# Performance work log

Measured on AMD Instinct MI355X. Metric: run time of the kernel, lower is better.

## Reference

```python
import jax, jax.numpy as jnp
import numpy as np
import math

B, T, NEURAL = 8, 8192, 256
D, H, L, FF = 1024, 16, 8, 4096
HD = D // H
KLEN = 14
BLANK = 41
DIP = 40
INTER = 3
GKS, GSIG = 20, 2.0
DAYS = 24


def _gauss_kernel():
    x = np.arange(GKS, dtype=np.float32)
    mean = (GKS - 1) / 2
    k = np.exp(-(((x - mean) / GSIG) ** 2) / 2) / (GSIG * math.sqrt(2 * math.pi))
    k = k / k.sum()
    return jnp.asarray(np.tile(k[None, None, :], (NEURAL, 1, 1)))  # [C,1,K]


def _ln(x, w, b, eps=1e-5):
    mu = jnp.mean(x, axis=-1, keepdims=True)
    xc = x - mu
    var = jnp.mean(xc * xc, axis=-1, keepdims=True)
    return xc * jax.lax.rsqrt(var + eps) * w + b


def setup_inputs() -> dict:
    key = jax.random.key(0)
    ks = iter(jax.random.split(key, 64))
    def nrm(shape, s=0.02):
        return jax.random.normal(next(ks), shape, jnp.float32) * s
    PE_IN = KLEN * NEURAL
    return {
        "neural": jax.random.normal(next(ks), (B, T, NEURAL), jnp.float32),
        "lengths": jax.random.randint(next(ks), (B,), 1, T + 1),
        "day_idx": jax.random.randint(next(ks), (B,), 0, DAYS),
        "day_W": jnp.broadcast_to(jnp.eye(NEURAL, dtype=jnp.float32), (DAYS, NEURAL, NEURAL)) + nrm((DAYS, NEURAL, NEURAL), 0.01),
        "day_b": jnp.zeros((DAYS, 1, NEURAL), jnp.float32),
        "pe_ln1_w": jnp.ones((PE_IN,), jnp.float32),
        "pe_ln1_b": jnp.zeros((PE_IN,), jnp.float32),
        "pe_W": nrm((PE_IN, D)),
        "pe_b": jnp.zeros((D,), jnp.float32),
        "pe_ln2_w": jnp.ones((D,), jnp.float32),
        "pe_ln2_b": jnp.zeros((D,), jnp.float32),
        "ln_attn_w": jnp.ones((L, D), jnp.float32),
        "ln_attn_b": jnp.zeros((L, D), jnp.float32),
        "qkv_W": nrm((L, D, 3 * D)),
        "qkv_b": jnp.zeros((L, 3 * D), jnp.float32),
        "attn_out_W": nrm((L, D, D)),
        "attn_out_b": jnp.zeros((L, D), jnp.float32),
        "ff_ln_w": jnp.ones((L, D), jnp.float32),
        "ff_ln_b": jnp.zeros((L, D), jnp.float32),
        "fc1_W": nrm((L, D, FF)),
        "fc1_b": jnp.zeros((L, FF), jnp.float32),
        "fc2_W": nrm((L, FF, D)),
        "fc2_b": jnp.zeros((L, D), jnp.float32),
        "final_ln_w": jnp.ones((D,), jnp.float32),
        "final_ln_b": jnp.zeros((D,), jnp.float32),
        "ih_W": nrm((D, BLANK)),
        "ih_b": jnp.zeros((BLANK,), jnp.float32),
        "fb_W": nrm((BLANK, D)),
        "fb_b": jnp.zeros((D,), jnp.float32),
        "fh_W": nrm((D, BLANK)),
        "fh_b": jnp.zeros((BLANK,), jnp.float32),
        "dh_W": nrm((D, DIP * DIP)),
        "dh_b": jnp.zeros((DIP * DIP,), jnp.float32),
    }


def reference(neural, lengths, day_idx, day_W, day_b, pe_ln1_w, pe_ln1_b, pe_W, pe_b, pe_ln2_w, pe_ln2_b, ln_attn_w, ln_attn_b, qkv_W, qkv_b, attn_out_W, attn_out_b, ff_ln_w, ff_ln_b, fc1_W, fc1_b, fc2_W, fc2_b, final_ln_w, final_ln_b, ih_W, ih_b, fb_W, fb_b, fh_W, fh_b, dh_W, dh_b):
    # --- depthwise gaussian smoothing along time (even kernel -> length T+1, as torch) ---
    x = jnp.transpose(neural, (0, 2, 1))  # [B, C, T]
    x = jax.lax.conv_general_dilated(x, _gauss_kernel(), (1,), [(GKS // 2, GKS // 2)],
                                     dimension_numbers=("NCH", "OIH", "NCH"),
                                     feature_group_count=NEURAL)
    x = jnp.transpose(x, (0, 2, 1))  # [B, T+1, C]
    # --- day-specific linear + softsign + length mask ---
    x = jnp.einsum("btd,bdk->btk", x, day_W[day_idx]) + day_b[day_idx]
    x = x / (1.0 + jnp.abs(x))  # Softsign
    Tm = x.shape[1]
    pm = jnp.arange(Tm)[None, :] >= lengths[:, None]
    x = jnp.where(pm[:, :, None], 0.0, x)
    # --- patch embedding ---
    npatch = Tm // KLEN
    x = x[:, : npatch * KLEN, :].reshape(B, npatch, KLEN * NEURAL)
    x = _ln(x, pe_ln1_w, pe_ln1_b, 1e-6)
    x = x @ pe_W + pe_b
    x = _ln(x, pe_ln2_w, pe_ln2_b, 1e-6)
    S = npatch
    causal = jnp.triu(jnp.full((S, S), -1e9, dtype=x.dtype), 1)
    eff = jnp.maximum(lengths // KLEN, 1)
    pad = jnp.arange(S)[None, :] >= eff[:, None]  # [B, S]
    scale = 1.0 / math.sqrt(HD)
    h = x
    inter_lp = None
    for i in range(L):
        a = _ln(h, ln_attn_w[i], ln_attn_b[i])
        qkv = a @ qkv_W[i] + qkv_b[i]
        q, k, v = jnp.split(qkv, 3, axis=-1)
        q = q.reshape(B, S, H, HD).transpose(0, 2, 1, 3)
        k = k.reshape(B, S, H, HD).transpose(0, 2, 1, 3)
        v = v.reshape(B, S, H, HD).transpose(0, 2, 1, 3)
        sc = jnp.einsum("bhqd,bhkd->bhqk", q, k) * scale + causal
        sc = jnp.where(pad[:, None, None, :], -1e30, sc)
        att = jax.nn.softmax(sc, axis=-1)
        o = jnp.einsum("bhqk,bhkd->bhqd", att, v).transpose(0, 2, 1, 3).reshape(B, S, D)
        o = o @ attn_out_W[i] + attn_out_b[i]
        o = jnp.where(pad[:, :, None], 0.0, o)
        h = h + o
        f = _ln(h, ff_ln_w[i], ff_ln_b[i])
        f = jax.nn.gelu(f @ fc1_W[i] + fc1_b[i], approximate=False) @ fc2_W[i] + fc2_b[i]
        h = h + f
        if i == INTER:
            inter_lp = jax.nn.log_softmax(h @ ih_W + ih_b, axis=-1)
            h = h + (jnp.exp(inter_lp) @ fb_W + fb_b)  # feedback projection
    h = _ln(h, final_ln_w, final_ln_b)
    final_lp = jax.nn.log_softmax(h @ fh_W + fh_b, axis=-1)
    # --- diphone marginalization ---
    lp = jax.nn.log_softmax(h @ dh_W + dh_b, axis=-1).reshape(B, S, DIP, DIP)
    left = jax.scipy.special.logsumexp(lp, axis=3)
    right = jax.scipy.special.logsumexp(lp, axis=2)
    comb = jnp.logaddexp(left, right) - math.log(2.0)
    comb = comb - jax.scipy.special.logsumexp(comb, axis=-1, keepdims=True)
    return final_lp, inter_lp, comb
```

## Files before the change

### kernel.cpp

```cpp
#include <hip/hip_runtime.h>
#include <math.h>

#define Bz    8
#define Tt    8192
#define NEU   256
#define Dm    1024
#define Hh    16
#define Ll    8
#define FFd   4096
#define HDd   64
#define KL    14
#define BLANK 41
#define DIPd  40
#define GKS   20
#define TmD   8193
#define Ss    585
#define PEIN  3584
#define MTOK  (Bz * Ss)
#define SpV   608
#define TCH   128

#define NEG_INF (-3.4e38f)

typedef __attribute__((ext_vector_type(8))) short short8;
typedef __attribute__((ext_vector_type(4))) float f32x4;
typedef unsigned short ushort_t;

__device__ __forceinline__ float bf2f(ushort_t u) {
  union { unsigned int i; float f; } v; v.i = ((unsigned int)u) << 16; return v.f;
}
__device__ __forceinline__ ushort_t f2bf(float f) {
  union { float f; unsigned int i; } v; v.f = f;
  unsigned int x = v.i;
  if ((x & 0x7fffffffu) > 0x7f800000u) return 0x7fc0;
  return (ushort_t)((x + 0x7fffu + ((x >> 16) & 1u)) >> 16);
}

__global__ __launch_bounds__(256) void smooth_kernel(
    const float* __restrict__ neural, float* __restrict__ out) {
  const int b = blockIdx.y, c = threadIdx.x;
  const int t0 = blockIdx.x * TCH;
  float w[GKS];
  float wsum = 0.f;
#pragma unroll
  for (int j = 0; j < GKS; j++) {
    float e = (j - 9.5f) * 0.5f;
    w[j] = expf(-0.5f * e * e);
    wsum += w[j];
  }
  const float inv = 1.f / wsum;
#pragma unroll
  for (int j = 0; j < GKS; j++) w[j] *= inv;

  const float* src = neural + (size_t)b * Tt * NEU + c;
  float* dst = out + ((size_t)b * TmD + t0) * NEU + c;

  float win[GKS];
#pragma unroll
  for (int j = 0; j < GKS; j++) {
    const int tt = t0 - GKS / 2 + j;
    win[j] = (tt >= 0 && tt < Tt) ? src[(size_t)tt * NEU] : 0.f;
  }
  const int nt = min(TCH, TmD - t0);
  for (int t = 0; t < nt; t++) {
    const int tt = t0 + t + GKS / 2;
    const float nv = (tt < Tt) ? src[(size_t)tt * NEU] : 0.f;
    float acc = 0.f;
#pragma unroll
    for (int j = 0; j < GKS; j++) acc += win[j] * w[j];
    dst[(size_t)t * NEU] = acc;
#pragma unroll
    for (int j = 0; j < GKS - 1; j++) win[j] = win[j + 1];
    win[GKS - 1] = nv;
  }
}

#define DROWS 16
__global__ __launch_bounds__(256) void day_kernel(
    float* __restrict__ x, const float* __restrict__ dayW,
    const float* __restrict__ dayB, const int* __restrict__ day_idx,
    const int* __restrict__ lengths) {
  const int b = blockIdx.y;
  const int t0 = blockIdx.x * DROWS;
  const int c = threadIdx.x;
  const int di = day_idx[b];
  const int len = lengths[b];
  const float* W = dayW + (size_t)di * NEU * NEU;
  __shared__ float rows[DROWS][NEU];
  float* xb = x + ((size_t)b * TmD + t0) * NEU;
  const int nr = min(DROWS, TmD - t0);
  for (int r = 0; r < nr; r++) rows[r][c] = xb[(size_t)r * NEU + c];
  __syncthreads();
  float acc[DROWS];
  const float bb = dayB[(size_t)di * NEU + c];
#pragma unroll
  for (int r = 0; r < DROWS; r++) acc[r] = bb;
  for (int d = 0; d < NEU; d++) {
    const float w = W[(size_t)d * NEU + c];
#pragma unroll
    for (int r = 0; r < DROWS; r++) acc[r] += rows[r][d] * w;
  }
  for (int r = 0; r < nr; r++) {
    const int t = t0 + r;
    float v = acc[r] / (1.f + fabsf(acc[r]));
    xb[(size_t)r * NEU + c] = (t < len) ? v : 0.f;
  }
}

__global__ __launch_bounds__(256) void ln_kernel(
    const float* __restrict__ in, const float* __restrict__ w,
    const float* __restrict__ bias, float* __restrict__ dstf,
    ushort_t* __restrict__ dstb,
    int N, float eps, int inner, long strideA, long strideB) {
  const int row = blockIdx.x;
  const float* src = in + (size_t)(row / inner) * strideA + (size_t)(row % inner) * strideB;
  const int tid = threadIdx.x;
  float s = 0.f, ss = 0.f;
  for (int i = tid; i < N; i += 256) {
    float v = src[i];
    s += v; ss += v * v;
  }
  __shared__ float rs[256], rss[256];
  rs[tid] = s; rss[tid] = ss;
  __syncthreads();
  for (int k = 128; k > 0; k >>= 1) {
    if (tid < k) { rs[tid] += rs[tid + k]; rss[tid] += rss[tid + k]; }
    __syncthreads();
  }
  const float mean = rs[0] / N;
  const float var = rss[0] / N - mean * mean;
  const float rstd = rsqrtf(var + eps);
  for (int i = tid; i < N; i += 256) {
    const float r = (src[i] - mean) * rstd * w[i] + bias[i];
    if (dstf) dstf[(size_t)row * N + i] = r;
    else dstb[(size_t)row * N + i] = f2bf(r);
  }
}

__global__ __launch_bounds__(256) void convt_kernel(
    const float* __restrict__ in, ushort_t* __restrict__ out,
    int R, int C, int Rp) {
  __shared__ float t[32][33];
  const int r0 = blockIdx.x * 32, c0 = blockIdx.y * 32;
  const int tx = threadIdx.x, ty = threadIdx.y;
#pragma unroll
  for (int i = 0; i < 4; i++) {
    const int r = r0 + ty + i * 8, c = c0 + tx;
    t[ty + i * 8][tx] = (r < R && c < C) ? in[(size_t)r * C + c] : 0.f;
  }
  __syncthreads();
#pragma unroll
  for (int i = 0; i < 4; i++) {
    const int c = c0 + ty + i * 8, r = r0 + tx;
    if (c < C && r < Rp) out[(size_t)c * Rp + r] = f2bf(t[tx][ty + i * 8]);
  }
}

__global__ __launch_bounds__(256) void f2b_kernel(
    const float* __restrict__ in, ushort_t* __restrict__ out, int n) {
  for (int i = blockIdx.x * 256 + threadIdx.x; i < n; i += gridDim.x * 256)
    out[i] = f2bf(in[i]);
}

#define BM 128
#define BN 128
#define BKh 32
__global__ __launch_bounds__(256) void gemm_bf16(
    const ushort_t* __restrict__ A, const ushort_t* __restrict__ Bt,
    const float* __restrict__ bias, float* __restrict__ Cf,
    ushort_t* __restrict__ Cb, int M, int N, int K, int epi,
    const int* __restrict__ eff) {
  __shared__ short As[BM * BKh];
  __shared__ short Bs[BN * BKh];
  const int tid = threadIdx.x;
  const int wave = tid >> 6, lane = tid & 63;
  const int lm = lane & 15, quad = lane >> 4;
  const int bm = blockIdx.x * BM, bn = blockIdx.y * BN;
  const int wm = (wave >> 1) * 64, wn = (wave & 1) * 64;

  f32x4 acc[4][4] = {};

  const int ldrow = lane >> 2;
  const int ldk = (lane & 3) * 8;

  for (int k0 = 0; k0 < K; k0 += BKh) {
#pragma unroll
    for (int r = 0; r < 4; r++) {
      const int cid = wave * 4 + r;
      if (cid < 8) {
        int row = bm + cid * 16 + ldrow;
        row = min(row, M - 1);
        const ushort_t* gp = A + (size_t)row * K + k0 + ldk;
        __builtin_amdgcn_global_load_lds(
            (const __attribute__((address_space(1))) unsigned int*)gp,
            (__attribute__((address_space(3))) unsigned int*)((char*)As + cid * 1024),
            16, 0, 0);
      } else {
        int row = bn + (cid - 8) * 16 + ldrow;
        row = min(row, N - 1);
        const ushort_t* gp = Bt + (size_t)row * K + k0 + ldk;
        __builtin_amdgcn_global_load_lds(
            (const __attribute__((address_space(1))) unsigned int*)gp,
            (__attribute__((address_space(3))) unsigned int*)((char*)Bs + (cid - 8) * 1024),
            16, 0, 0);
      }
    }
    __syncthreads();
    short8 af[4], bf[4];
#pragma unroll
    for (int mt = 0; mt < 4; mt++)
      af[mt] = *(const short8*)&As[(wm + mt * 16 + lm) * BKh + quad * 8];
#pragma unroll
    for (int nt = 0; nt < 4; nt++)
      bf[nt] = *(const short8*)&Bs[(wn + nt * 16 + lm) * BKh + quad * 8];
#pragma unroll
    for (int mt = 0; mt < 4; mt++)
#pragma unroll
      for (int nt = 0; nt < 4; nt++)
        acc[mt][nt] = __builtin_amdgcn_mfma_f32_16x16x32_bf16(
            af[mt], bf[nt], acc[mt][nt], 0, 0, 0);
    __syncthreads();
  }

#pragma unroll
  for (int mt = 0; mt < 4; mt++) {
#pragma unroll
    for (int r = 0; r < 4; r++) {
      const int gm = bm + wm + mt * 16 + quad * 4 + r;
      if (gm >= M) continue;
      bool masked = false;
      if (epi == 3) masked = ((gm % Ss) >= eff[gm / Ss]);
#pragma unroll
      for (int nt = 0; nt < 4; nt++) {
        const int gn = bn + wn + nt * 16 + lm;
        if (gn >= N) continue;
        const float v = acc[mt][nt][r] + bias[gn];
        const size_t o = (size_t)gm * N + gn;
        if (epi == 0) Cf[o] = v;
        else if (epi == 1) Cb[o] = f2bf(0.5f * v * (1.f + erff(v * 0.70710678118654752f)));
        else if (epi == 2) Cf[o] += v;
        else if (epi == 3) { if (!masked) Cf[o] += v; }
        else Cb[o] = f2bf(v);
      }
    }
  }
}

__global__ __launch_bounds__(256) void vt_kernel(
    const ushort_t* __restrict__ qkv, ushort_t* __restrict__ vt) {
  __shared__ ushort_t t[32][33];
  const int s0 = blockIdx.x * 32;
  const int h = blockIdx.y >> 1, d0 = (blockIdx.y & 1) * 32;
  const int b = blockIdx.z;
  const int tx = threadIdx.x, ty = threadIdx.y;
#pragma unroll
  for (int i = 0; i < 4; i++) {
    const int s = s0 + ty + i * 8;
    t[ty + i * 8][tx] = (s < Ss)
        ? qkv[((size_t)(b * Ss + s) * 3 + 2) * Dm + h * HDd + d0 + tx]
        : (ushort_t)0;
  }
  __syncthreads();
#pragma unroll
  for (int i = 0; i < 4; i++) {
    const int d = d0 + ty + i * 8;
    vt[((size_t)(b * Hh + h) * HDd + d) * SpV + s0 + tx] = t[tx][ty + i * 8];
  }
}

__global__ __launch_bounds__(256) void fattn_kernel(
    const ushort_t* __restrict__ qkv, const ushort_t* __restrict__ vt,
    ushort_t* __restrict__ out, const int* __restrict__ eff) {
  const int wave = threadIdx.x >> 6, lane = threadIdx.x & 63;
  const int lm = lane & 15, quad = lane >> 4;
  const int nQT = (Ss + 15) / 16;
  const int qt = ((int)gridDim.x - 1 - (int)blockIdx.x) * 4 + wave;
  if (qt >= nQT) return;
  const int h = blockIdx.y, b = blockIdx.z;
  const int e = eff[b];
  __shared__ ushort_t pl[4][16][40];
  const int q0 = qt * 16;

  const int qrow = min(q0 + lm, Ss - 1);
  const short8* qp = (const short8*)(qkv + (size_t)(b * Ss + qrow) * 3 * Dm + h * HDd + quad * 8);
  const short8 aq0 = qp[0], aq1 = qp[4];

  f32x4 acc[4] = {};
  float mrow[4], lrow[4];
#pragma unroll
  for (int r = 0; r < 4; r++) { mrow[r] = NEG_INF; lrow[r] = 0.f; }

  const int kmax = min(q0 + 15, e - 1);
  const int ntiles = (kmax >> 5) + 1;

  for (int kt = 0; kt < ntiles; kt++) {
    const int k0 = kt * 32;
    f32x4 s0 = {}, s1 = {};
    {
      const int c = min(k0 + lm, Ss - 1);
      const short8* kp = (const short8*)(qkv + ((size_t)(b * Ss + c) * 3 + 1) * Dm + h * HDd + quad * 8);
      s0 = __builtin_amdgcn_mfma_f32_16x16x32_bf16(aq0, kp[0], s0, 0, 0, 0);
      s0 = __builtin_amdgcn_mfma_f32_16x16x32_bf16(aq1, kp[4], s0, 0, 0, 0);
    }
    {
      const int c = min(k0 + 16 + lm, Ss - 1);
      const short8* kp = (const short8*)(qkv + ((size_t)(b * Ss + c) * 3 + 1) * Dm + h * HDd + quad * 8);
      s1 = __builtin_amdgcn_mfma_f32_16x16x32_bf16(aq0, kp[0], s1, 0, 0, 0);
      s1 = __builtin_amdgcn_mfma_f32_16x16x32_bf16(aq1, kp[4], s1, 0, 0, 0);
    }
    float sv0[4], sv1[4], tm[4];
#pragma unroll
    for (int r = 0; r < 4; r++) {
      const int row = q0 + quad * 4 + r;
      const int jm = min(row, e - 1);
      sv0[r] = (k0 + lm <= jm) ? s0[r] * 0.125f : NEG_INF;
      sv1[r] = (k0 + 16 + lm <= jm) ? s1[r] * 0.125f : NEG_INF;
      tm[r] = fmaxf(sv0[r], sv1[r]);
    }
#pragma unroll
    for (int off = 8; off; off >>= 1)
#pragma unroll
      for (int r = 0; r < 4; r++) tm[r] = fmaxf(tm[r], __shfl_xor(tm[r], off));
    float ps[4];
#pragma unroll
    for (int r = 0; r < 4; r++) {
      const float nm = fmaxf(mrow[r], tm[r]);
      const float sc = expf(mrow[r] - nm);
      mrow[r] = nm;
      const float p0 = expf(sv0[r] - nm);
      const float p1 = expf(sv1[r] - nm);
      sv0[r] = p0; sv1[r] = p1;
      ps[r] = p0 + p1;
      lrow[r] *= sc;
#pragma unroll
      for (int nt = 0; nt < 4; nt++) acc[nt][r] *= sc;
    }
#pragma unroll
    for (int off = 8; off; off >>= 1)
#pragma unroll
      for (int r = 0; r < 4; r++) ps[r] += __shfl_xor(ps[r], off);
#pragma unroll
    for (int r = 0; r < 4; r++) {
      lrow[r] += ps[r];
      pl[wave][quad * 4 + r][lm] = f2bf(sv0[r]);
      pl[wave][quad * 4 + r][16 + lm] = f2bf(sv1[r]);
    }
    const short8 pf = *(const short8*)&pl[wave][lm][quad * 8];
    const ushort_t* vtb = vt + (size_t)(b * Hh + h) * HDd * SpV + k0 + quad * 8;
#pragma unroll
    for (int nt = 0; nt < 4; nt++) {
      const short8 vf = *(const short8*)(vtb + (size_t)(nt * 16 + lm) * SpV);
      acc[nt] = __builtin_amdgcn_mfma_f32_16x16x32_bf16(pf, vf, acc[nt], 0, 0, 0);
    }
  }

#pragma unroll
  for (int r = 0; r < 4; r++) {
    const int row = q0 + quad * 4 + r;
    if (row >= Ss) continue;
    const float inv = 1.f / lrow[r];
#pragma unroll
    for (int nt = 0; nt < 4; nt++)
      out[(size_t)(b * Ss + row) * Dm + h * HDd + nt * 16 + lm] = f2bf(acc[nt][r] * inv);
  }
}

__global__ __launch_bounds__(64) void lsm41_kernel(
    const float* __restrict__ in, float* __restrict__ lp,
    ushort_t* __restrict__ probs) {
  const int row = blockIdx.x, t = threadIdx.x;
  const float z = (t < BLANK) ? in[(size_t)row * BLANK + t] : NEG_INF;
  float m = z;
#pragma unroll
  for (int off = 32; off; off >>= 1) m = fmaxf(m, __shfl_xor(m, off));
  float s = (t < BLANK) ? expf(z - m) : 0.f;
#pragma unroll
  for (int off = 32; off; off >>= 1) s += __shfl_xor(s, off);
  const float l = z - m - logf(s);
  if (t < BLANK) lp[(size_t)row * BLANK + t] = l;
  if (probs) probs[(size_t)row * 64 + t] = (t < BLANK) ? f2bf(expf(l)) : 0;
}

__global__ __launch_bounds__(64) void diphone_kernel(
    const float* __restrict__ in, float* __restrict__ out) {
  __shared__ float z[DIPd * DIPd];
  __shared__ float u[DIPd];
  const int row = blockIdx.x, t = threadIdx.x;
  for (int i = t; i < DIPd * DIPd; i += 64) z[i] = in[(size_t)row * (DIPd * DIPd) + i];
  __syncthreads();
  if (t < DIPd) {
    float m1 = NEG_INF;
    for (int j = 0; j < DIPd; j++) m1 = fmaxf(m1, z[t * DIPd + j]);
    float s1 = 0.f;
    for (int j = 0; j < DIPd; j++) s1 += expf(z[t * DIPd + j] - m1);
    const float lr = m1 + logf(s1);
    float m2 = NEG_INF;
    for (int j = 0; j < DIPd; j++) m2 = fmaxf(m2, z[j * DIPd + t]);
    float s2 = 0.f;
    for (int j = 0; j < DIPd; j++) s2 += expf(z[j * DIPd + t] - m2);
    const float lc = m2 + logf(s2);
    const float mx = fmaxf(lr, lc), mn = fminf(lr, lc);
    u[t] = mx + log1pf(expf(mn - mx));
  }
  __syncthreads();
  const float v = (t < DIPd) ? u[t] : NEG_INF;
  float m = v;
#pragma unroll
  for (int off = 32; off; off >>= 1) m = fmaxf(m, __shfl_xor(m, off));
  float s = (t < DIPd) ? expf(v - m) : 0.f;
#pragma unroll
  for (int off = 32; off; off >>= 1) s += __shfl_xor(s, off);
  const float lse = m + logf(s);
  if (t < DIPd) out[(size_t)row * DIPd + t] = v - lse;
}

__global__ void eff_kernel(const int* __restrict__ lengths, int* __restrict__ eff) {
  const int t = threadIdx.x;
  if (t < Bz) {
    int e = lengths[t] / KL;
    eff[t] = e < 1 ? 1 : e;
  }
}

extern "C" void kernel_launch(void* const* d_in, const int* in_sizes, int n_in,
                              void* d_out, int out_size, void* d_ws, size_t ws_size,
                              hipStream_t stream) {
  (void)in_sizes; (void)n_in; (void)out_size; (void)ws_size;
  const float* neural     = (const float*)d_in[0];
  const int*   lengths    = (const int*)d_in[1];
  const int*   day_idx    = (const int*)d_in[2];
  const float* day_W      = (const float*)d_in[3];
  const float* day_b      = (const float*)d_in[4];
  const float* pe_ln1_w   = (const float*)d_in[5];
  const float* pe_ln1_b   = (const float*)d_in[6];
  const float* pe_W       = (const float*)d_in[7];
  const float* pe_b       = (const float*)d_in[8];
  const float* pe_ln2_w   = (const float*)d_in[9];
  const float* pe_ln2_b   = (const float*)d_in[10];
  const float* ln_attn_w  = (const float*)d_in[11];
  const float* ln_attn_b  = (const float*)d_in[12];
  const float* qkv_W      = (const float*)d_in[13];
  const float* qkv_b      = (const float*)d_in[14];
  const float* attn_out_W = (const float*)d_in[15];
  const float* attn_out_b = (const float*)d_in[16];
  const float* ff_ln_w    = (const float*)d_in[17];
  const float* ff_ln_b    = (const float*)d_in[18];
  const float* fc1_W      = (const float*)d_in[19];
  const float* fc1_b      = (const float*)d_in[20];
  const float* fc2_W      = (const float*)d_in[21];
  const float* fc2_b      = (const float*)d_in[22];
  const float* final_ln_w = (const float*)d_in[23];
  const float* final_ln_b = (const float*)d_in[24];
  const float* ih_W       = (const float*)d_in[25];
  const float* ih_b       = (const float*)d_in[26];
  const float* fb_W       = (const float*)d_in[27];
  const float* fb_b       = (const float*)d_in[28];
  const float* fh_W       = (const float*)d_in[29];
  const float* fh_b       = (const float*)d_in[30];
  const float* dh_W       = (const float*)d_in[31];
  const float* dh_b       = (const float*)d_in[32];

  float* out = (float*)d_out;
  char* p = (char*)d_ws;

  float*    buf_x    = (float*)p;          p += 67117056;
  ushort_t* buf_pein = (ushort_t*)p;
  ushort_t* buf_qkv  = (ushort_t*)p;       p += 33546240;
  float*    buf_h    = (float*)p;          p += 19169280;
  ushort_t* buf_abf  = (ushort_t*)p;       p += 9584640;
  ushort_t* buf_ao   = (ushort_t*)p;       p += 9584640;
  char*     ffp      = p;                  p += 38338560;
  ushort_t* wbuf     = (ushort_t*)p;       p += 25380864;
  int*      eff      = (int*)p;            p += 32;

  ushort_t* buf_ff   = (ushort_t*)ffp;
  float*    buf_dip  = (float*)ffp;
  float*    buf_blank= (float*)(ffp + 29952000);
  ushort_t* buf_probs= (ushort_t*)(ffp + 30719520);
  float*    buf_peout= buf_x;
  ushort_t* buf_vt   = (ushort_t*)buf_x;

  ushort_t* qkvT = wbuf;
  ushort_t* aoT  = wbuf + 3145728;
  ushort_t* fc1T = wbuf + 4194304;
  ushort_t* fc2T = wbuf + 8388608;
  ushort_t* ihT  = wbuf + 12582912;
  ushort_t* fbT  = wbuf + 12624896;
  ushort_t* peT  = wbuf;
  ushort_t* dhT  = wbuf;
  ushort_t* fhT  = wbuf + 1638400;

  auto convt = [&](const float* in, ushort_t* o, int R, int C, int Rp) {
    dim3 g((Rp + 31) / 32, (C + 31) / 32);
    convt_kernel<<<g, dim3(32, 8), 0, stream>>>(in, o, R, C, Rp);
  };
  auto gemm = [&](const ushort_t* A, const ushort_t* Bt, const float* bias,
                  float* Cf, ushort_t* Cb, int M_, int N_, int K_, int epi) {
    dim3 g((M_ + BM - 1) / BM, (N_ + BN - 1) / BN);
    gemm_bf16<<<g, 256, 0, stream>>>(A, Bt, bias, Cf, Cb, M_, N_, K_, epi, eff);
  };

  eff_kernel<<<1, 64, 0, stream>>>(lengths, eff);
  smooth_kernel<<<dim3((TmD + TCH - 1) / TCH, Bz), 256, 0, stream>>>(neural, buf_x);
  day_kernel<<<dim3((TmD + DROWS - 1) / DROWS, Bz), 256, 0, stream>>>(buf_x, day_W, day_b, day_idx, lengths);

  ln_kernel<<<MTOK, 256, 0, stream>>>(buf_x, pe_ln1_w, pe_ln1_b, nullptr, buf_pein,
                                      PEIN, 1e-6f, Ss, (long)TmD * NEU, (long)KL * NEU);
  convt(pe_W, peT, PEIN, Dm, PEIN);
  convt(ih_W, ihT, Dm, BLANK, Dm);
  convt(fb_W, fbT, BLANK, Dm, 64);
  gemm(buf_pein, peT, pe_b, buf_peout, nullptr, MTOK, Dm, PEIN, 0);
  ln_kernel<<<MTOK, 256, 0, stream>>>(buf_peout, pe_ln2_w, pe_ln2_b, buf_h, nullptr,
                                      Dm, 1e-6f, MTOK, 0L, (long)Dm);

  const int nQT = (Ss + 15) / 16;
  const int fgx = (nQT + 3) / 4;

  for (int i = 0; i < Ll; i++) {
    convt(qkv_W + (size_t)i * Dm * 3 * Dm, qkvT, Dm, 3 * Dm, Dm);
    convt(attn_out_W + (size_t)i * Dm * Dm, aoT, Dm, Dm, Dm);
    convt(fc1_W + (size_t)i * Dm * FFd, fc1T, Dm, FFd, Dm);
    convt(fc2_W + (size_t)i * FFd * Dm, fc2T, FFd, Dm, FFd);

    ln_kernel<<<MTOK, 256, 0, stream>>>(buf_h, ln_attn_w + (size_t)i * Dm,
                                        ln_attn_b + (size_t)i * Dm, nullptr, buf_abf,
                                        Dm, 1e-5f, MTOK, 0L, (long)Dm);
    gemm(buf_abf, qkvT, qkv_b + (size_t)i * 3 * Dm, nullptr, buf_qkv,
         MTOK, 3 * Dm, Dm, 4);
    vt_kernel<<<dim3(SpV / 32, Hh * 2, Bz), dim3(32, 8), 0, stream>>>(buf_qkv, buf_vt);
    fattn_kernel<<<dim3(fgx, Hh, Bz), 256, 0, stream>>>(buf_qkv, buf_vt, buf_ao, eff);
    gemm(buf_ao, aoT, attn_out_b + (size_t)i * Dm, buf_h, nullptr,
         MTOK, Dm, Dm, 3);
    ln_kernel<<<MTOK, 256, 0, stream>>>(buf_h, ff_ln_w + (size_t)i * Dm,
                                        ff_ln_b + (size_t)i * Dm, nullptr, buf_abf,
                                        Dm, 1e-5f, MTOK, 0L, (long)Dm);
    gemm(buf_abf, fc1T, fc1_b + (size_t)i * FFd, nullptr, buf_ff,
         MTOK, FFd, Dm, 1);
    gemm(buf_ff, fc2T, fc2_b + (size_t)i * Dm, buf_h, nullptr,
         MTOK, Dm, FFd, 2);
    if (i == 3) {
      f2b_kernel<<<1024, 256, 0, stream>>>(buf_h, buf_abf, MTOK * Dm);
      gemm(buf_abf, ihT, ih_b, buf_blank, nullptr, MTOK, BLANK, Dm, 0);
      lsm41_kernel<<<MTOK, 64, 0, stream>>>(buf_blank, out + (size_t)MTOK * BLANK, buf_probs);
      gemm(buf_probs, fbT, fb_b, buf_h, nullptr, MTOK, Dm, 64, 2);
    }
  }

  ln_kernel<<<MTOK, 256, 0, stream>>>(buf_h, final_ln_w, final_ln_b, nullptr, buf_abf,
                                      Dm, 1e-5f, MTOK, 0L, (long)Dm);
  convt(dh_W, dhT, Dm, DIPd * DIPd, Dm);
  convt(fh_W, fhT, Dm, BLANK, Dm);
  gemm(buf_abf, fhT, fh_b, buf_blank, nullptr, MTOK, BLANK, Dm, 0);
  lsm41_kernel<<<MTOK, 64, 0, stream>>>(buf_blank, out, nullptr);
  gemm(buf_abf, dhT, dh_b, buf_dip, nullptr, MTOK, DIPd * DIPd, Dm, 0);
  diphone_kernel<<<MTOK, 64, 0, stream>>>(buf_dip, out + (size_t)2 * MTOK * BLANK);
}
```

Before: 5.030 ms.

## Run the day-specific linear transform on bf16 MFMA with hi/lo activation split

```diff
diff --git a/kernel.cpp b/kernel.cpp
--- a/kernel.cpp
+++ b/kernel.cpp
@@ -24,6 +24,7 @@
 
 typedef __attribute__((ext_vector_type(8))) short short8;
 typedef __attribute__((ext_vector_type(4))) float f32x4;
+typedef __attribute__((ext_vector_type(4))) unsigned short us4;
 typedef unsigned short ushort_t;
 
 __device__ __forceinline__ float bf2f(ushort_t u) {
@@ -75,36 +76,104 @@
   }
 }
 
-#define DROWS 16
-__global__ __launch_bounds__(256) void day_kernel(
-    float* __restrict__ x, const float* __restrict__ dayW,
+__global__ __launch_bounds__(256) void dayt_kernel(
+    const float* __restrict__ dayW, const int* __restrict__ day_idx,
+    ushort_t* __restrict__ out) {
+  __shared__ float t[32][33];
+  const int b = blockIdx.z;
+  const int k0 = blockIdx.x * 32, c0 = blockIdx.y * 32;
+  const int tx = threadIdx.x, ty = threadIdx.y;
+  const float* W = dayW + (size_t)day_idx[b] * NEU * NEU;
+#pragma unroll
+  for (int i = 0; i < 4; i++)
+    t[ty + i * 8][tx] = W[(size_t)(k0 + ty + i * 8) * NEU + c0 + tx];
+  __syncthreads();
+  ushort_t* o = out + (size_t)b * NEU * NEU;
+#pragma unroll
+  for (int i = 0; i < 4; i++)
+    o[(size_t)(c0 + ty + i * 8) * NEU + k0 + tx] = f2bf(t[tx][ty + i * 8]);
+}
+
+#define DBM 64
+#define DBK 32
+__global__ __launch_bounds__(256) void day_mfma(
+    float* __restrict__ x, const ushort_t* __restrict__ Wt,
     const float* __restrict__ dayB, const int* __restrict__ day_idx,
     const int* __restrict__ lengths) {
   const int b = blockIdx.y;
-  const int t0 = blockIdx.x * DROWS;
-  const int c = threadIdx.x;
+  const int bm = blockIdx.x * DBM;
+  const int tid = threadIdx.x;
+  const int wave = tid >> 6, lane = tid & 63;
+  const int lm = lane & 15, quad = lane >> 4;
   const int di = day_idx[b];
   const int len = lengths[b];
-  const float* W = dayW + (size_t)di * NEU * NEU;
-  __shared__ float rows[DROWS][NEU];
-  float* xb = x + ((size_t)b * TmD + t0) * NEU;
-  const int nr = min(DROWS, TmD - t0);
-  for (int r = 0; r < nr; r++) rows[r][c] = xb[(size_t)r * NEU + c];
-  __syncthreads();
-  float acc[DROWS];
-  const float bb = dayB[(size_t)di * NEU + c];
-#pragma unroll
-  for (int r = 0; r < DROWS; r++) acc[r] = bb;
-  for (int d = 0; d < NEU; d++) {
-    const float w = W[(size_t)d * NEU + c];
-#pragma unroll
-    for (int r = 0; r < DROWS; r++) acc[r] += rows[r][d] * w;
-  }
-  for (int r = 0; r < nr; r++) {
-    const int t = t0 + r;
-    float v = acc[r] / (1.f + fabsf(acc[r]));
-    xb[(size_t)r * NEU + c] = (t < len) ? v : 0.f;
-  }
+  __shared__ ushort_t Ahi[DBM][40], Alo[DBM][40], Bs[256][40];
+  f32x4 acc[4][4] = {};
+  const float* xb = x + (size_t)b * TmD * NEU;
+  const ushort_t* wt = Wt + (size_t)b * NEU * NEU;
+
+  for (int k0 = 0; k0 < NEU; k0 += DBK) {
+    __syncthreads();
+#pragma unroll
+    for (int i = 0; i < 2; i++) {
+      const int f = tid + i * 256;
+      const int row = f >> 3, kq = f & 7;
+      const int gr = min(bm + row, TmD - 1);
+      const float4 v = *(const float4*)&xb[(size_t)gr * NEU + k0 + kq * 4];
+      const float vv[4] = {v.x, v.y, v.z, v.w};
+      us4 hv, lv;
+#pragma unroll
+      for (int j = 0; j < 4; j++) {
+        union { float f; unsigned int u; } uu; uu.f = vv[j];
+        const ushort_t h = (ushort_t)(uu.u >> 16);
+        hv[j] = h;
+        lv[j] = f2bf(vv[j] - bf2f(h));
+      }
+      *(us4*)&Ahi[row][kq * 4] = hv;
+      *(us4*)&Alo[row][kq * 4] = lv;
+    }
+#pragma unroll
+    for (int i = 0; i < 4; i++) {
+      const int u = tid + i * 256;
+      const int c = u >> 2, kq8 = u & 3;
+      const short8 wv = *(const short8*)&wt[(size_t)c * NEU + k0 + kq8 * 8];
+      *(short8*)&Bs[c][kq8 * 8] = wv;
+    }
+    __syncthreads();
+    short8 ah[4], al[4], bfr[4];
+#pragma unroll
+    for (int mt = 0; mt < 4; mt++) {
+      ah[mt] = *(const short8*)&Ahi[mt * 16 + lm][quad * 8];
+      al[mt] = *(const short8*)&Alo[mt * 16 + lm][quad * 8];
+    }
+#pragma unroll
+    for (int nt = 0; nt < 4; nt++)
+      bfr[nt] = *(const short8*)&Bs[wave * 64 + nt * 16 + lm][quad * 8];
+#pragma unroll
+    for (int mt = 0; mt < 4; mt++)
+#pragma unroll
+      for (int nt = 0; nt < 4; nt++) {
+        acc[mt][nt] = __builtin_amdgcn_mfma_f32_16x16x32_bf16(
+            ah[mt], bfr[nt], acc[mt][nt], 0, 0, 0);
+        acc[mt][nt] = __builtin_amdgcn_mfma_f32_16x16x32_bf16(
+            al[mt], bfr[nt], acc[mt][nt], 0, 0, 0);
+      }
+  }
+
+#pragma unroll
+  for (int mt = 0; mt < 4; mt++)
+#pragma unroll
+    for (int r = 0; r < 4; r++) {
+      const int gm = bm + mt * 16 + quad * 4 + r;
+      if (gm >= TmD) continue;
+#pragma unroll
+      for (int nt = 0; nt < 4; nt++) {
+        const int gn = wave * 64 + nt * 16 + lm;
+        float v = acc[mt][nt][r] + dayB[(size_t)di * NEU + gn];
+        v = v / (1.f + fabsf(v));
+        x[((size_t)b * TmD + gm) * NEU + gn] = (gm < len) ? v : 0.f;
+      }
+    }
 }
 
 __global__ __launch_bounds__(256) void ln_kernel(
@@ -479,6 +548,7 @@
   ushort_t* buf_probs= (ushort_t*)(ffp + 30719520);
   float*    buf_peout= buf_x;
   ushort_t* buf_vt   = (ushort_t*)buf_x;
+  ushort_t* dayWt    = buf_ao;
 
   ushort_t* qkvT = wbuf;
   ushort_t* aoT  = wbuf + 3145728;
@@ -501,8 +571,9 @@
   };
 
   eff_kernel<<<1, 64, 0, stream>>>(lengths, eff);
+  dayt_kernel<<<dim3(8, 8, Bz), dim3(32, 8), 0, stream>>>(day_W, day_idx, dayWt);
   smooth_kernel<<<dim3((TmD + TCH - 1) / TCH, Bz), 256, 0, stream>>>(neural, buf_x);
-  day_kernel<<<dim3((TmD + DROWS - 1) / DROWS, Bz), 256, 0, stream>>>(buf_x, day_W, day_b, day_idx, lengths);
+  day_mfma<<<dim3((TmD + DBM - 1) / DBM, Bz), 256, 0, stream>>>(buf_x, dayWt, day_b, day_idx, lengths);
 
   ln_kernel<<<MTOK, 256, 0, stream>>>(buf_x, pe_ln1_w, pe_ln1_b, nullptr, buf_pein,
                                       PEIN, 1e-6f, Ss, (long)TmD * NEU, (long)KL * NEU);
```

Result: faster. 4.771 ms (-5.2%).
